# Kernel tuning notes

Measured on AMD Instinct MI355X. Metric: run time of the kernel, lower is better.

## Reference

```python
import jax, jax.numpy as jnp
import numpy as np

QDIM = 32
H = 512
B = 65536
BIAS = 2.0
N_TRIL = QDIM * (QDIM + 1) // 2  # 528 total params per sample
TRIL_R, TRIL_C = np.tril_indices(QDIM, -1)  # strictly-lower entries (500)
DIAG = np.arange(QDIM)


def setup_inputs() -> dict:
    key = jax.random.key(0)
    ks = jax.random.split(key, 12)
    def lin(k, fan_in, fan_out):
        return jax.random.normal(k, (fan_in, fan_out), dtype=jnp.float32) / np.sqrt(fan_in).astype(np.float32)
    return {
        "q": jax.random.normal(ks[0], (B, QDIM), dtype=jnp.float32),
        # ResMLP embed: input linear, two residual hidden blocks, output linear
        "W_in": lin(ks[1], QDIM, H), "b_in": jnp.zeros((H,), jnp.float32),
        "W_h1": lin(ks[2], H, H),    "b_h1": jnp.zeros((H,), jnp.float32),
        "W_h2": lin(ks[3], H, H),    "b_h2": jnp.zeros((H,), jnp.float32),
        "W_out": lin(ks[4], H, H),   "b_out": jnp.zeros((H,), jnp.float32),
        # Cholesky parameter head: H -> qdim*(qdim+1)/2
        "W_o": lin(ks[5], H, N_TRIL), "b_o": jnp.zeros((N_TRIL,), jnp.float32),
    }


def reference(q, W_in, b_in, W_h1, b_h1, W_h2, b_h2, W_out, b_out, W_o, b_o):
    # ResMLP embed (relu, residual connections on equal-width hidden layers)
    x = jax.nn.relu(q @ W_in + b_in)               # [B, H]
    x = jax.nn.relu(x @ W_h1 + b_h1) + x           # residual block 1
    x = jax.nn.relu(x @ W_h2 + b_h2) + x           # residual block 2
    embed = x @ W_out + b_out                      # [B, H]
    # Cholesky factor params
    L_params = embed @ W_o + b_o                   # [B, 528]
    L_diag = L_params[:, :QDIM] + BIAS             # [B, 32]
    L_tril = L_params[:, QDIM:]                    # [B, 496+... strictly lower]
    Bsz = q.shape[0]
    L = jnp.zeros((Bsz, QDIM, QDIM), L_params.dtype)
    L = L.at[:, TRIL_R, TRIL_C].set(L_tril)        # bfill_lowertriangle
    L = L.at[:, DIAG, DIAG].set(L_diag)            # bfill_diagonal
    M = L @ jnp.swapaxes(L, -1, -2)                # SPD mass matrix [B, 32, 32]
    return M
```

## Files before the change

### kernel.cpp

```cpp
#include <hip/hip_runtime.h>
#include <math.h>

typedef __bf16 bf16;
typedef bf16 bf16x2 __attribute__((ext_vector_type(2)));
typedef bf16 bf16x4 __attribute__((ext_vector_type(4)));
typedef bf16 bf16x8 __attribute__((ext_vector_type(8)));
typedef float f32x4 __attribute__((ext_vector_type(4)));

#define BATCH 65536
#define QD 32
#define HD 512
#define NT 528
#define BM 64
#define BIAS_C 2.0f

#define OFF_WIN  0
#define OFF_WH1  16384
#define OFF_WH2  278528
#define OFF_WOUT 540672
#define OFF_WO   802816
#define WT_TOTAL 1073152
#define N_TILES  2096

#define MFMA(a, b, c) __builtin_amdgcn_mfma_f32_16x16x32_bf16((a), (b), (c), 0, 0, 0)

__global__ __launch_bounds__(256) void prep_weights(
    const float* __restrict__ W_in, const float* __restrict__ W_h1,
    const float* __restrict__ W_h2, const float* __restrict__ W_out,
    const float* __restrict__ W_o, bf16* __restrict__ wt)
{
    const int bt = blockIdx.x;

    __shared__ float lds[32][17];
    const float* src; int ld, nt, kt;
    if (bt < 32)        { src = W_in;                 nt = bt;     kt = 0;      ld = HD; }
    else if (bt < 544)  { int t = bt - 32;   src = W_h1;  nt = t >> 4; kt = t & 15; ld = HD; }
    else if (bt < 1056) { int t = bt - 544;  src = W_h2;  nt = t >> 4; kt = t & 15; ld = HD; }
    else if (bt < 1568) { int t = bt - 1056; src = W_out; nt = t >> 4; kt = t & 15; ld = HD; }
    else                { int t = bt - 1568; src = W_o;   nt = t >> 4; kt = t & 15; ld = NT; }

    const int s = threadIdx.x * 2;
    {
        int ki = s >> 4, fi = s & 15;
        const float* p = src + (size_t)(kt * 32 + ki) * ld + nt * 16 + fi;
        lds[ki][fi]     = p[0];
        lds[ki][fi + 1] = p[1];
    }
    __syncthreads();
    {
        int fi = s >> 5, ki = s & 31;
        bf16x2 w;
        w[0] = (bf16)lds[ki][fi];
        w[1] = (bf16)lds[ki + 1][fi];
        *(bf16x2*)(wt + (size_t)bt * 512 + s) = w;
    }
}

__device__ __forceinline__ int xbyte(int m, int f) {
    return m * 1024 + ((((f >> 3)) ^ m) << 4) + ((f & 7) << 1);
}

__device__ __forceinline__ int lbyte(int il, int r, int c) {
    return il * 2048 + r * 64 + ((((c >> 3)) ^ (r & 3) ^ (il & 3)) << 4) + ((c & 7) << 1);
}

__device__ __forceinline__ void writeL2(unsigned char* smem, int il, int r_, int c_, float v) {
    bf16 hi = (bf16)v;
    bf16 lo = (bf16)(v - (float)hi);
    int off = lbyte(il, r_, c_);
    *(bf16*)(smem + off) = hi;
    *(bf16*)(smem + 32768 + off) = lo;
}

__device__ __forceinline__ void p2rc(int p, int& r_, int& c_) {
    if (p < QD) { r_ = p; c_ = p; }
    else {
        int t = p - QD;
        r_ = (int)((1.0f + sqrtf(8.0f * (float)t + 1.0f)) * 0.5f);
        while (r_ * (r_ - 1) / 2 > t) --r_;
        while ((r_ + 1) * r_ / 2 <= t) ++r_;
        c_ = t - r_ * (r_ - 1) / 2;
    }
}

__global__ __launch_bounds__(1024, 4) void fused_kernel(
    const float* __restrict__ q,
    const float* __restrict__ b_in, const float* __restrict__ b_h1,
    const float* __restrict__ b_h2, const float* __restrict__ b_out,
    const float* __restrict__ b_o,
    const bf16* __restrict__ wt, float* __restrict__ out)
{
    __shared__ __attribute__((aligned(16))) unsigned char smem[65536];
    const int tid  = threadIdx.x;
    const int lane = tid & 63;
    const int wave = tid >> 6;
    const int l15  = lane & 15;
    const int quad = lane >> 4;
    const int blk  = blockIdx.x;

    const f32x4 zf = {0.f, 0.f, 0.f, 0.f};
    f32x4 acc[2][4];

    {
        bf16x8 bfr[4];
        #pragma unroll
        for (int ct = 0; ct < 4; ++ct) {
            const float* qp = q + (size_t)(blk * 64 + ct * 16 + l15) * QD + quad * 8;
            f32x4 lo = *(const f32x4*)qp;
            f32x4 hi = *(const f32x4*)(qp + 4);
            bf16x8 b;
            #pragma unroll
            for (int j = 0; j < 4; ++j) { b[j] = (bf16)lo[j]; b[4 + j] = (bf16)hi[j]; }
            bfr[ct] = b;
        }
        #pragma unroll
        for (int rt = 0; rt < 2; ++rt) {
            bf16x8 a = *(const bf16x8*)(wt + OFF_WIN + (wave * 2 + rt) * 512 + l15 * 32 + quad * 8);
            #pragma unroll
            for (int ct = 0; ct < 4; ++ct)
                acc[rt][ct] = MFMA(a, bfr[ct], zf);
        }
        #pragma unroll
        for (int rt = 0; rt < 2; ++rt) {
            int f0 = wave * 32 + rt * 16 + quad * 4;
            f32x4 bias = *(const f32x4*)(b_in + f0);
            #pragma unroll
            for (int ct = 0; ct < 4; ++ct) {
                int m = ct * 16 + l15;
                bf16x4 w;
                #pragma unroll
                for (int r = 0; r < 4; ++r) {
                    float v = acc[rt][ct][r] + bias[r];
                    v = v > 0.f ? v : 0.f;
                    w[r] = (bf16)v;
                }
                *(bf16x4*)(smem + xbyte(m, f0)) = w;
            }
        }
    }
    __syncthreads();

    const bf16*  WL[3] = { wt + OFF_WH1, wt + OFF_WH2, wt + OFF_WOUT };
    const float* BL[3] = { b_h1, b_h2, b_out };
    #pragma unroll
    for (int L = 0; L < 3; ++L) {
        #pragma unroll
        for (int rt = 0; rt < 2; ++rt)
            #pragma unroll
            for (int ct = 0; ct < 4; ++ct)
                acc[rt][ct] = zf;
        const bf16* W = WL[L];
        #pragma unroll 2
        for (int kk = 0; kk < 16; ++kk) {
            bf16x8 bfr2[4];
            #pragma unroll
            for (int ct = 0; ct < 4; ++ct) {
                int m = ct * 16 + l15;
                bfr2[ct] = *(const bf16x8*)(smem + m * 1024 + (((kk * 4 + quad) ^ m) << 4));
            }
            #pragma unroll
            for (int rt = 0; rt < 2; ++rt) {
                bf16x8 a = *(const bf16x8*)(W + ((wave * 2 + rt) * 16 + kk) * 512 + l15 * 32 + quad * 8);
                #pragma unroll
                for (int ct = 0; ct < 4; ++ct)
                    acc[rt][ct] = MFMA(a, bfr2[ct], acc[rt][ct]);
            }
        }
        __syncthreads();
        {
            const float* Bv = BL[L];
            #pragma unroll
            for (int rt = 0; rt < 2; ++rt) {
                int f0 = wave * 32 + rt * 16 + quad * 4;
                f32x4 bias = *(const f32x4*)(Bv + f0);
                #pragma unroll
                for (int ct = 0; ct < 4; ++ct) {
                    int m = ct * 16 + l15;
                    unsigned char* p = smem + xbyte(m, f0);
                    bf16x4 w;
                    if (L < 2) {
                        bf16x4 old = *(const bf16x4*)p;
                        #pragma unroll
                        for (int r = 0; r < 4; ++r) {
                            float v = acc[rt][ct][r] + bias[r];
                            v = v > 0.f ? v : 0.f;
                            v += (float)old[r];
                            w[r] = (bf16)v;
                        }
                    } else {
                        #pragma unroll
                        for (int r = 0; r < 4; ++r) {
                            float v = acc[rt][ct][r] + bias[r];
                            w[r] = (bf16)v;
                        }
                    }
                    *(bf16x4*)p = w;
                }
            }
        }
        __syncthreads();
    }

    f32x4 acc_ex = zf;
    #pragma unroll
    for (int rt = 0; rt < 2; ++rt)
        #pragma unroll
        for (int ct = 0; ct < 4; ++ct)
            acc[rt][ct] = zf;
    #pragma unroll 2
    for (int kk = 0; kk < 16; ++kk) {
        bf16x8 bfr2[4];
        #pragma unroll
        for (int ct = 0; ct < 4; ++ct) {
            int m = ct * 16 + l15;
            bfr2[ct] = *(const bf16x8*)(smem + m * 1024 + (((kk * 4 + quad) ^ m) << 4));
        }
        #pragma unroll
        for (int rt = 0; rt < 2; ++rt) {
            bf16x8 a = *(const bf16x8*)(wt + OFF_WO + ((wave * 2 + rt) * 16 + kk) * 512 + l15 * 32 + quad * 8);
            #pragma unroll
            for (int ct = 0; ct < 4; ++ct)
                acc[rt][ct] = MFMA(a, bfr2[ct], acc[rt][ct]);
        }
        if (wave >= 8 && wave < 12) {
            bf16x8 aex = *(const bf16x8*)(wt + OFF_WO + (32 * 16 + kk) * 512 + l15 * 32 + quad * 8);
            if (wave == 8) acc_ex = MFMA(aex, bfr2[0], acc_ex);
            else if (wave == 9) acc_ex = MFMA(aex, bfr2[1], acc_ex);
            else if (wave == 10) acc_ex = MFMA(aex, bfr2[2], acc_ex);
            else acc_ex = MFMA(aex, bfr2[3], acc_ex);
        }
    }
    __syncthreads();

    f32x4 bo4[2];
    #pragma unroll
    for (int rt = 0; rt < 2; ++rt)
        bo4[rt] = *(const f32x4*)(b_o + wave * 32 + rt * 16 + quad * 4);
    f32x4 bo_ex = zf;
    if (wave >= 8 && wave < 12) bo_ex = *(const f32x4*)(b_o + 512 + quad * 4);

    int rcr[2][4], rcc[2][4];
    #pragma unroll
    for (int rt = 0; rt < 2; ++rt)
        #pragma unroll
        for (int r = 0; r < 4; ++r)
            p2rc(wave * 32 + rt * 16 + quad * 4 + r, rcr[rt][r], rcc[rt][r]);
    int rex[4], cex[4];
    if (wave >= 8 && wave < 12) {
        #pragma unroll
        for (int r = 0; r < 4; ++r)
            p2rc(512 + quad * 4 + r, rex[r], cex[r]);
    }

    {
        unsigned long long* z = (unsigned long long*)smem;
        #pragma unroll
        for (int i = 0; i < 8; ++i) z[tid + 1024 * i] = 0ull;
    }
    __syncthreads();

    #pragma unroll
    for (int g = 0; g < 4; ++g) {
        const int il = l15;
        #pragma unroll
        for (int rt = 0; rt < 2; ++rt) {
            #pragma unroll
            for (int r = 0; r < 4; ++r) {
                float v = acc[rt][g][r] + bo4[rt][r];
                if (wave == 0) v += BIAS_C;
                writeL2(smem, il, rcr[rt][r], rcc[rt][r], v);
            }
        }
        if (wave == 8 + g) {
            #pragma unroll
            for (int r = 0; r < 4; ++r)
                writeL2(smem, il, rex[r], cex[r], acc_ex[r] + bo_ex[r]);
        }
        __syncthreads();
        {
            const int it = wave;
            bf16x8 Fh[2], Fl[2];
            #pragma unroll
            for (int tl = 0; tl < 2; ++tl) {
                int m = tl * 16 + l15;
                int ch = quad ^ (m & 3) ^ (it & 3);
                int off = it * 2048 + m * 64 + (ch << 4);
                Fh[tl] = *(const bf16x8*)(smem + off);
                Fl[tl] = *(const bf16x8*)(smem + 32768 + off);
            }
            long base = ((long)(blk * 64 + g * 16 + it)) * 1024;
            #pragma unroll
            for (int mt = 0; mt < 2; ++mt) {
                #pragma unroll
                for (int nt = 0; nt < 2; ++nt) {
                    f32x4 mm = MFMA(Fh[mt], Fh[nt], zf);
                    mm = MFMA(Fh[mt], Fl[nt], mm);
                    mm = MFMA(Fl[mt], Fh[nt], mm);
                    #pragma unroll
                    for (int r = 0; r < 4; ++r)
                        out[base + (long)(mt * 16 + quad * 4 + r) * 32 + nt * 16 + l15] = mm[r];
                }
            }
        }
        __syncthreads();
    }
}

extern "C" void kernel_launch(void* const* d_in, const int* in_sizes, int n_in,
                              void* d_out, int out_size, void* d_ws, size_t ws_size,
                              hipStream_t stream)
{
    const float* q     = (const float*)d_in[0];
    const float* W_in  = (const float*)d_in[1];
    const float* b_in  = (const float*)d_in[2];
    const float* W_h1  = (const float*)d_in[3];
    const float* b_h1  = (const float*)d_in[4];
    const float* W_h2  = (const float*)d_in[5];
    const float* b_h2  = (const float*)d_in[6];
    const float* W_out = (const float*)d_in[7];
    const float* b_out = (const float*)d_in[8];
    const float* W_o   = (const float*)d_in[9];
    const float* b_o   = (const float*)d_in[10];
    float* out = (float*)d_out;
    bf16* wt = (bf16*)d_ws;

    prep_weights<<<N_TILES, 256, 0, stream>>>(W_in, W_h1, W_h2, W_out, W_o, wt);
    fused_kernel<<<BATCH / BM, 1024, 0, stream>>>(q, b_in, b_h1, b_h2, b_out, b_o, wt, out);
}
```

Measured before the change: 480.8 us.

## Halve block to 512 threads with four row tiles per wave

Each block now runs 8 waves instead of 16, and each wave computes four 16-row feature tiles instead of two. Every B fragment read from LDS therefore feeds twice as many MFMAs, and the final Gram stage loops twice per wave. The triangular index mapping is precomputed into LDS byte offsets, and the bias is folded into the accumulators before the store loop. This cuts LDS traffic per MFMA and the per-element index work, at the cost of higher register pressure and fewer waves per CU to hide latency.

```diff
diff --git a/kernel.cpp b/kernel.cpp
--- a/kernel.cpp
+++ b/kernel.cpp
@@ -62,14 +62,6 @@
 
 __device__ __forceinline__ int lbyte(int il, int r, int c) {
     return il * 2048 + r * 64 + ((((c >> 3)) ^ (r & 3) ^ (il & 3)) << 4) + ((c & 7) << 1);
-}
-
-__device__ __forceinline__ void writeL2(unsigned char* smem, int il, int r_, int c_, float v) {
-    bf16 hi = (bf16)v;
-    bf16 lo = (bf16)(v - (float)hi);
-    int off = lbyte(il, r_, c_);
-    *(bf16*)(smem + off) = hi;
-    *(bf16*)(smem + 32768 + off) = lo;
 }
 
 __device__ __forceinline__ void p2rc(int p, int& r_, int& c_) {
@@ -83,7 +75,7 @@
     }
 }
 
-__global__ __launch_bounds__(1024, 4) void fused_kernel(
+__global__ __launch_bounds__(512, 4) void fused_kernel(
     const float* __restrict__ q,
     const float* __restrict__ b_in, const float* __restrict__ b_h1,
     const float* __restrict__ b_h2, const float* __restrict__ b_out,
@@ -99,7 +91,7 @@
     const int blk  = blockIdx.x;
 
     const f32x4 zf = {0.f, 0.f, 0.f, 0.f};
-    f32x4 acc[2][4];
+    f32x4 acc[4][4];
 
     {
         bf16x8 bfr[4];
@@ -114,15 +106,15 @@
             bfr[ct] = b;
         }
         #pragma unroll
-        for (int rt = 0; rt < 2; ++rt) {
-            bf16x8 a = *(const bf16x8*)(wt + OFF_WIN + (wave * 2 + rt) * 512 + l15 * 32 + quad * 8);
+        for (int rt = 0; rt < 4; ++rt) {
+            bf16x8 a = *(const bf16x8*)(wt + OFF_WIN + (wave * 4 + rt) * 512 + l15 * 32 + quad * 8);
             #pragma unroll
             for (int ct = 0; ct < 4; ++ct)
                 acc[rt][ct] = MFMA(a, bfr[ct], zf);
         }
         #pragma unroll
-        for (int rt = 0; rt < 2; ++rt) {
-            int f0 = wave * 32 + rt * 16 + quad * 4;
+        for (int rt = 0; rt < 4; ++rt) {
+            int f0 = wave * 64 + rt * 16 + quad * 4;
             f32x4 bias = *(const f32x4*)(b_in + f0);
             #pragma unroll
             for (int ct = 0; ct < 4; ++ct) {
@@ -145,7 +137,7 @@
     #pragma unroll
     for (int L = 0; L < 3; ++L) {
         #pragma unroll
-        for (int rt = 0; rt < 2; ++rt)
+        for (int rt = 0; rt < 4; ++rt)
             #pragma unroll
             for (int ct = 0; ct < 4; ++ct)
                 acc[rt][ct] = zf;
@@ -159,8 +151,8 @@
                 bfr2[ct] = *(const bf16x8*)(smem + m * 1024 + (((kk * 4 + quad) ^ m) << 4));
             }
             #pragma unroll
-            for (int rt = 0; rt < 2; ++rt) {
-                bf16x8 a = *(const bf16x8*)(W + ((wave * 2 + rt) * 16 + kk) * 512 + l15 * 32 + quad * 8);
+            for (int rt = 0; rt < 4; ++rt) {
+                bf16x8 a = *(const bf16x8*)(W + ((wave * 4 + rt) * 16 + kk) * 512 + l15 * 32 + quad * 8);
                 #pragma unroll
                 for (int ct = 0; ct < 4; ++ct)
                     acc[rt][ct] = MFMA(a, bfr2[ct], acc[rt][ct]);
@@ -170,8 +162,8 @@
         {
             const float* Bv = BL[L];
             #pragma unroll
-            for (int rt = 0; rt < 2; ++rt) {
-                int f0 = wave * 32 + rt * 16 + quad * 4;
+            for (int rt = 0; rt < 4; ++rt) {
+                int f0 = wave * 64 + rt * 16 + quad * 4;
                 f32x4 bias = *(const f32x4*)(Bv + f0);
                 #pragma unroll
                 for (int ct = 0; ct < 4; ++ct) {
@@ -203,7 +195,7 @@
 
     f32x4 acc_ex = zf;
     #pragma unroll
-    for (int rt = 0; rt < 2; ++rt)
+    for (int rt = 0; rt < 4; ++rt)
         #pragma unroll
         for (int ct = 0; ct < 4; ++ct)
             acc[rt][ct] = zf;
@@ -216,69 +208,96 @@
             bfr2[ct] = *(const bf16x8*)(smem + m * 1024 + (((kk * 4 + quad) ^ m) << 4));
         }
         #pragma unroll
-        for (int rt = 0; rt < 2; ++rt) {
-            bf16x8 a = *(const bf16x8*)(wt + OFF_WO + ((wave * 2 + rt) * 16 + kk) * 512 + l15 * 32 + quad * 8);
+        for (int rt = 0; rt < 4; ++rt) {
+            bf16x8 a = *(const bf16x8*)(wt + OFF_WO + ((wave * 4 + rt) * 16 + kk) * 512 + l15 * 32 + quad * 8);
             #pragma unroll
             for (int ct = 0; ct < 4; ++ct)
                 acc[rt][ct] = MFMA(a, bfr2[ct], acc[rt][ct]);
         }
-        if (wave >= 8 && wave < 12) {
+        if (wave >= 4) {
             bf16x8 aex = *(const bf16x8*)(wt + OFF_WO + (32 * 16 + kk) * 512 + l15 * 32 + quad * 8);
-            if (wave == 8) acc_ex = MFMA(aex, bfr2[0], acc_ex);
-            else if (wave == 9) acc_ex = MFMA(aex, bfr2[1], acc_ex);
-            else if (wave == 10) acc_ex = MFMA(aex, bfr2[2], acc_ex);
+            if (wave == 4) acc_ex = MFMA(aex, bfr2[0], acc_ex);
+            else if (wave == 5) acc_ex = MFMA(aex, bfr2[1], acc_ex);
+            else if (wave == 6) acc_ex = MFMA(aex, bfr2[2], acc_ex);
             else acc_ex = MFMA(aex, bfr2[3], acc_ex);
         }
     }
     __syncthreads();
 
-    f32x4 bo4[2];
-    #pragma unroll
-    for (int rt = 0; rt < 2; ++rt)
-        bo4[rt] = *(const f32x4*)(b_o + wave * 32 + rt * 16 + quad * 4);
-    f32x4 bo_ex = zf;
-    if (wave >= 8 && wave < 12) bo_ex = *(const f32x4*)(b_o + 512 + quad * 4);
-
-    int rcr[2][4], rcc[2][4];
-    #pragma unroll
-    for (int rt = 0; rt < 2; ++rt)
-        #pragma unroll
-        for (int r = 0; r < 4; ++r)
-            p2rc(wave * 32 + rt * 16 + quad * 4 + r, rcr[rt][r], rcc[rt][r]);
-    int rex[4], cex[4];
-    if (wave >= 8 && wave < 12) {
-        #pragma unroll
-        for (int r = 0; r < 4; ++r)
-            p2rc(512 + quad * 4 + r, rex[r], cex[r]);
+    #pragma unroll
+    for (int rt = 0; rt < 4; ++rt) {
+        f32x4 b = *(const f32x4*)(b_o + wave * 64 + rt * 16 + quad * 4);
+        if (rt < 2 && wave == 0) {
+            #pragma unroll
+            for (int r = 0; r < 4; ++r) b[r] += BIAS_C;
+        }
+        #pragma unroll
+        for (int ct = 0; ct < 4; ++ct)
+            #pragma unroll
+            for (int r = 0; r < 4; ++r)
+                acc[rt][ct][r] += b[r];
+    }
+    if (wave >= 4) {
+        f32x4 be = *(const f32x4*)(b_o + 512 + quad * 4);
+        #pragma unroll
+        for (int r = 0; r < 4; ++r) acc_ex[r] += be[r];
+    }
+
+    int loff[4][4];
+    #pragma unroll
+    for (int rt = 0; rt < 4; ++rt)
+        #pragma unroll
+        for (int r = 0; r < 4; ++r) {
+            int rr, cc;
+            p2rc(wave * 64 + rt * 16 + quad * 4 + r, rr, cc);
+            loff[rt][r] = lbyte(l15, rr, cc);
+        }
+    int loffex[4] = {0, 0, 0, 0};
+    if (wave >= 4) {
+        #pragma unroll
+        for (int r = 0; r < 4; ++r) {
+            int rr, cc;
+            p2rc(512 + quad * 4 + r, rr, cc);
+            loffex[r] = lbyte(l15, rr, cc);
+        }
     }
 
     {
         unsigned long long* z = (unsigned long long*)smem;
         #pragma unroll
-        for (int i = 0; i < 8; ++i) z[tid + 1024 * i] = 0ull;
+        for (int i = 0; i < 16; ++i) z[tid + 512 * i] = 0ull;
     }
     __syncthreads();
 
     #pragma unroll
     for (int g = 0; g < 4; ++g) {
-        const int il = l15;
-        #pragma unroll
-        for (int rt = 0; rt < 2; ++rt) {
+        #pragma unroll
+        for (int rt = 0; rt < 4; ++rt) {
             #pragma unroll
             for (int r = 0; r < 4; ++r) {
-                float v = acc[rt][g][r] + bo4[rt][r];
-                if (wave == 0) v += BIAS_C;
-                writeL2(smem, il, rcr[rt][r], rcc[rt][r], v);
-            }
-        }
-        if (wave == 8 + g) {
-            #pragma unroll
-            for (int r = 0; r < 4; ++r)
-                writeL2(smem, il, rex[r], cex[r], acc_ex[r] + bo_ex[r]);
+                float v = acc[rt][g][r];
+                bf16 hi = (bf16)v;
+                bf16 lo = (bf16)(v - (float)hi);
+                int off = loff[rt][r];
+                *(bf16*)(smem + off) = hi;
+                *(bf16*)(smem + 32768 + off) = lo;
+            }
+        }
+        if (wave == 4 + g) {
+            #pragma unroll
+            for (int r = 0; r < 4; ++r) {
+                float v = acc_ex[r];
+                bf16 hi = (bf16)v;
+                bf16 lo = (bf16)(v - (float)hi);
+                int off = loffex[r];
+                *(bf16*)(smem + off) = hi;
+                *(bf16*)(smem + 32768 + off) = lo;
+            }
         }
         __syncthreads();
-        {
-            const int it = wave;
+        #pragma unroll
+        for (int ii = 0; ii < 2; ++ii) {
+            const int it = wave + ii * 8;
             bf16x8 Fh[2], Fl[2];
             #pragma unroll
             for (int tl = 0; tl < 2; ++tl) {
@@ -325,5 +344,5 @@
     bf16* wt = (bf16*)d_ws;
 
     prep_weights<<<N_TILES, 256, 0, stream>>>(W_in, W_h1, W_h2, W_out, W_o, wt);
-    fused_kernel<<<BATCH / BM, 1024, 0, stream>>>(q, b_in, b_h1, b_h2, b_out, b_o, wt, out);
-}
+    fused_kernel<<<BATCH / BM, 512, 0, stream>>>(q, b_in, b_h1, b_h2, b_out, b_o, wt, out);
+}
```

New measurement: 470.1 us. 2.2% less time.
